# Performance work log

Hardware: AMD Instinct MI355X
Metric: run time of the kernel (lower is better)

The kernel has to match this reference:

```python
import jax, jax.numpy as jnp
import numpy as np

DIM = 1024
HEADS = 16
MLP = 4096

def setup_inputs() -> dict:
    key = jax.random.key(0)
    ks = jax.random.split(key, 8)
    s = 0.02
    return {
        "x": jax.random.normal(ks[0], (4, 2048, DIM), dtype=jnp.float32),
        "W_qkv": jax.random.normal(ks[1], (DIM, 3 * DIM), dtype=jnp.float32) * s,
        "W_o": jax.random.normal(ks[2], (DIM, DIM), dtype=jnp.float32) * s,
        "b_o": jnp.zeros((DIM,), dtype=jnp.float32),
        "g1": jnp.ones((DIM,), dtype=jnp.float32),
        "be1": jnp.zeros((DIM,), dtype=jnp.float32),
        "W1": jax.random.normal(ks[3], (DIM, MLP), dtype=jnp.float32) * s,
        "b1": jnp.zeros((MLP,), dtype=jnp.float32),
        "W2": jax.random.normal(ks[4], (MLP, DIM), dtype=jnp.float32) * s,
        "b2": jnp.zeros((DIM,), dtype=jnp.float32),
        "g2": jnp.ones((DIM,), dtype=jnp.float32),
        "be2": jnp.zeros((DIM,), dtype=jnp.float32),
    }

def _gelu(x):
    # GELU approx used in source: x * sigmoid(1.702 * x)
    return x * jax.nn.sigmoid(1.702 * x)

def _layernorm(x, g, b, eps=1e-5):
    mu = jnp.mean(x, axis=-1, keepdims=True)
    var = jnp.var(x, axis=-1, keepdims=True)
    return (x - mu) * jax.lax.rsqrt(var + eps) * g + b

def reference(x, W_qkv, W_o, b_o, g1, be1, W1, b1, W2, b2, g2, be2):
    b, n, d = x.shape
    h = HEADS
    hd = d // h
    scale = hd ** -0.5
    qkv = x @ W_qkv                               # [b,n,3d]
    q, k, v = jnp.split(qkv, 3, axis=-1)
    q = q.reshape(b, n, h, hd).transpose(0, 2, 1, 3)  # [b,h,n,hd]
    k = k.reshape(b, n, h, hd).transpose(0, 2, 1, 3)
    v = v.reshape(b, n, h, hd).transpose(0, 2, 1, 3)
    dots = jnp.einsum('bhid,bhjd->bhij', q, k) * scale  # [b,h,n,n]
    attn = jax.nn.softmax(dots, axis=-1)
    out = jnp.einsum('bhij,bhjd->bhid', attn, v)
    out = out.transpose(0, 2, 1, 3).reshape(b, n, d)
    out = out @ W_o + b_o
    x = _layernorm(x + out, g1, be1)
    ff = _gelu(x @ W1 + b1) @ W2 + b2
    x = _layernorm(x + ff, g2, be2)
    return x
```

## Files before the change

kernel.cpp:

```cpp
#include <hip/hip_runtime.h>

typedef unsigned short u16;
typedef __attribute__((ext_vector_type(4))) float f32x4;
typedef __attribute__((ext_vector_type(8))) __bf16 bf16x8;
typedef __attribute__((ext_vector_type(8))) unsigned short u16x8;
typedef __attribute__((ext_vector_type(4))) unsigned short u16x4;

__device__ __forceinline__ u16 f2bf(float f) {
  __bf16 h = (__bf16)f;
  union { __bf16 h; u16 u; } v; v.h = h;
  return v.u;
}

__device__ __forceinline__ float bf2f(u16 u) {
  union { unsigned u; float f; } v; v.u = ((unsigned)u) << 16;
  return v.f;
}

__device__ __forceinline__ void async16(const void* g, void* l) {
  __builtin_amdgcn_global_load_lds(
      (const __attribute__((address_space(1))) unsigned int*)g,
      (__attribute__((address_space(3))) unsigned int*)l, 16, 0, 0);
}

__device__ __forceinline__ void barrier_f() {
  asm volatile("" ::: "memory");
  __builtin_amdgcn_s_barrier();
  asm volatile("" ::: "memory");
}

__global__ __launch_bounds__(256) void cvt_f32_bf16(const float* __restrict__ in,
                                                    u16* __restrict__ out, int n4) {
  int i = blockIdx.x * 256 + threadIdx.x;
  if (i >= n4) return;
  f32x4 v = *(const f32x4*)(in + (long)i * 4);
  u16x4 o;
#pragma unroll
  for (int j = 0; j < 4; j++) o[j] = f2bf(v[j]);
  *(u16x4*)(out + (long)i * 4) = o;
}

__global__ __launch_bounds__(256) void transpose_cvt(const float* __restrict__ W,
                                                     u16* __restrict__ Wt, int K, int N) {
  __shared__ float tile[32][33];
  int n0 = blockIdx.x * 32, k0 = blockIdx.y * 32;
  int tx = threadIdx.x & 31, ty = threadIdx.x >> 5;
#pragma unroll
  for (int i = 0; i < 32; i += 8)
    tile[ty + i][tx] = W[(long)(k0 + ty + i) * N + n0 + tx];
  __syncthreads();
#pragma unroll
  for (int i = 0; i < 32; i += 8)
    Wt[(long)(n0 + ty + i) * K + k0 + tx] = f2bf(tile[tx][ty + i]);
}

template <int BIAS, int GELU, int OBF, int QSCALE, int VW, int SPLITK>
__global__ __launch_bounds__(512, 1) void gemm8p(const u16* __restrict__ A,
                                                 const u16* __restrict__ Bt,
                                                 void* __restrict__ Cp,
                                                 const float* __restrict__ bias,
                                                 u16* __restrict__ vt,
                                                 int M, int N, int Kst, int Klen) {
  __shared__ u16 As[2][256 * 64];
  __shared__ u16 Bs[2][256 * 64];
  const int t = threadIdx.x, wid = t >> 6, ln = t & 63;
  const int lr = ln & 15, lg = ln >> 4;
  const int wr = wid >> 2, wc = wid & 3;

  const int gx = gridDim.x, gy = gridDim.y;
  const int nwg = gx * gy * gridDim.z;
  const int flat = (blockIdx.z * gy + blockIdx.y) * gx + blockIdx.x;
  const int cpx = nwg >> 3;
  const int swz = (flat & 7) * cpx + (flat >> 3);
  const int sx = swz % gx, rest = swz / gx;
  const int sy = rest % gy, sz = rest / gy;
  const int m0 = sy * 256, n0 = sx * 256;
  const long zo = (long)sz * Klen;
  const int NT = Klen >> 6;

  const int srow = t >> 3;
  const int sch = ((t & 7) ^ (srow & 7)) * 8;
  const u16* gA = A + (long)(m0 + srow) * Kst + zo + sch;
  const u16* gB = Bt + (long)(n0 + srow) * Kst + zo + sch;
  const long KL = Kst;

#define STAGE_A(tt, h)                                                     \
  {                                                                        \
    const u16* s_ = gA + (long)((h) * 128) * KL + (long)(tt) * 64;         \
    char* d_ = (char*)As + ((tt) & 1) * 32768 + (h) * 16384 + wid * 1024;  \
    async16(s_, d_);                                                       \
    async16(s_ + 64 * KL, d_ + 8192);                                      \
  }
#define STAGE_B(tt, h)                                                     \
  {                                                                        \
    const u16* s_ = gB + (long)((h) * 128) * KL + (long)(tt) * 64;         \
    char* d_ = (char*)Bs + ((tt) & 1) * 32768 + (h) * 16384 + wid * 1024;  \
    async16(s_, d_);                                                       \
    async16(s_ + 64 * KL, d_ + 8192);                                      \
  }

  f32x4 acc[8][4] = {};
  const int cx0 = (lg ^ (lr & 7)) * 16;
  const int cx1 = ((4 + lg) ^ (lr & 7)) * 16;

  STAGE_A(0, 0); STAGE_A(0, 1);
  STAGE_B(0, 0); STAGE_B(0, 1);
  STAGE_A(1, 0); STAGE_A(1, 1);

  for (int tK = 0; tK < NT; ++tK) {
    const int cur = tK & 1;
    const char* ldsA = (const char*)As + cur * 32768;
    const char* ldsB = (const char*)Bs + cur * 32768;
    if (tK == NT - 1) {
      asm volatile("s_waitcnt vmcnt(0)" ::: "memory");
    } else {
      asm volatile("s_waitcnt vmcnt(4)" ::: "memory");
    }
    barrier_f();

    bf16x8 aLo[4][2], aHi[4][2], bLo[2][2], bHi[2][2];
#pragma unroll
    for (int mf = 0; mf < 4; mf++) {
      int row = wr * 128 + mf * 16 + lr;
      aLo[mf][0] = *(const bf16x8*)(ldsA + row * 128 + cx0);
      aLo[mf][1] = *(const bf16x8*)(ldsA + row * 128 + cx1);
    }
#pragma unroll
    for (int nf = 0; nf < 2; nf++) {
      int row = wc * 64 + nf * 16 + lr;
      bLo[nf][0] = *(const bf16x8*)(ldsB + row * 128 + cx0);
      bLo[nf][1] = *(const bf16x8*)(ldsB + row * 128 + cx1);
    }
    if (tK + 1 < NT) STAGE_B(tK + 1, 0);
    barrier_f();
    __builtin_amdgcn_s_setprio(1);
#pragma unroll
    for (int mf = 0; mf < 4; mf++)
#pragma unroll
      for (int nf = 0; nf < 2; nf++) {
        acc[mf][nf] = __builtin_amdgcn_mfma_f32_16x16x32_bf16(aLo[mf][0], bLo[nf][0], acc[mf][nf], 0, 0, 0);
        acc[mf][nf] = __builtin_amdgcn_mfma_f32_16x16x32_bf16(aLo[mf][1], bLo[nf][1], acc[mf][nf], 0, 0, 0);
      }
    __builtin_amdgcn_s_setprio(0);
    barrier_f();

#pragma unroll
    for (int mf = 0; mf < 4; mf++) {
      int row = wr * 128 + (mf + 4) * 16 + lr;
      aHi[mf][0] = *(const bf16x8*)(ldsA + row * 128 + cx0);
      aHi[mf][1] = *(const bf16x8*)(ldsA + row * 128 + cx1);
    }
    if (tK + 1 < NT) STAGE_B(tK + 1, 1);
    barrier_f();
    __builtin_amdgcn_s_setprio(1);
#pragma unroll
    for (int mf = 0; mf < 4; mf++)
#pragma unroll
      for (int nf = 0; nf < 2; nf++) {
        acc[mf + 4][nf] = __builtin_amdgcn_mfma_f32_16x16x32_bf16(aHi[mf][0], bLo[nf][0], acc[mf + 4][nf], 0, 0, 0);
        acc[mf + 4][nf] = __builtin_amdgcn_mfma_f32_16x16x32_bf16(aHi[mf][1], bLo[nf][1], acc[mf + 4][nf], 0, 0, 0);
      }
    __builtin_amdgcn_s_setprio(0);
    barrier_f();

#pragma unroll
    for (int nf = 0; nf < 2; nf++) {
      int row = wc * 64 + (nf + 2) * 16 + lr;
      bHi[nf][0] = *(const bf16x8*)(ldsB + row * 128 + cx0);
      bHi[nf][1] = *(const bf16x8*)(ldsB + row * 128 + cx1);
    }
    if (tK + 2 < NT) STAGE_A(tK + 2, 0);
    barrier_f();
    __builtin_amdgcn_s_setprio(1);
#pragma unroll
    for (int mf = 0; mf < 4; mf++)
#pragma unroll
      for (int nf = 0; nf < 2; nf++) {
        acc[mf][nf + 2] = __builtin_amdgcn_mfma_f32_16x16x32_bf16(aLo[mf][0], bHi[nf][0], acc[mf][nf + 2], 0, 0, 0);
        acc[mf][nf + 2] = __builtin_amdgcn_mfma_f32_16x16x32_bf16(aLo[mf][1], bHi[nf][1], acc[mf][nf + 2], 0, 0, 0);
      }
    __builtin_amdgcn_s_setprio(0);
    barrier_f();

    if (tK + 2 < NT) STAGE_A(tK + 2, 1);
    barrier_f();
    __builtin_amdgcn_s_setprio(1);
#pragma unroll
    for (int mf = 0; mf < 4; mf++)
#pragma unroll
      for (int nf = 0; nf < 2; nf++) {
        acc[mf + 4][nf + 2] = __builtin_amdgcn_mfma_f32_16x16x32_bf16(aHi[mf][0], bHi[nf][0], acc[mf + 4][nf + 2], 0, 0, 0);
        acc[mf + 4][nf + 2] = __builtin_amdgcn_mfma_f32_16x16x32_bf16(aHi[mf][1], bHi[nf][1], acc[mf + 4][nf + 2], 0, 0, 0);
      }
    __builtin_amdgcn_s_setprio(0);
    barrier_f();
  }
#undef STAGE_A
#undef STAGE_B

  u16* const Cu = (u16*)Cp + (SPLITK ? (long)sz * M * N : 0);
#pragma unroll
  for (int mf = 0; mf < 8; mf++) {
    int rbase = m0 + wr * 128 + mf * 16 + lg * 4;
#pragma unroll
    for (int nf = 0; nf < 4; nf++) {
      int col = n0 + wc * 64 + nf * 16 + lr;
      float bv = BIAS ? bias[col] : 0.f;
      if (VW && col >= 2048) {
        int hd = col - 2048;
        int bq = rbase >> 11, key = rbase & 2047;
        u16x4 o4;
#pragma unroll
        for (int r = 0; r < 4; r++) o4[r] = f2bf(acc[mf][nf][r]);
        *(u16x4*)&vt[((long)(bq * 16 + (hd >> 6)) * 64 + (hd & 63)) * 2048 + key] = o4;
      } else if (SPLITK) {
#pragma unroll
        for (int r = 0; r < 4; r++)
          Cu[(long)(rbase + r) * N + col] = f2bf(acc[mf][nf][r]);
      } else {
#pragma unroll
        for (int r = 0; r < 4; r++) {
          float v = acc[mf][nf][r] + bv;
          if (GELU) v = v / (1.f + __expf(-1.702f * v));
          if (QSCALE && col < 1024) v *= 0.18033688011112043f;
          if (OBF) ((u16*)Cp)[(long)(rbase + r) * N + col] = f2bf(v);
          else ((float*)Cp)[(long)(rbase + r) * N + col] = v;
        }
      }
    }
  }
}

__global__ __launch_bounds__(512, 6) void attn_kernel(const u16* __restrict__ qkv,
                                                      const u16* __restrict__ vt,
                                                      u16* __restrict__ out) {
  const int b = blockIdx.y >> 4, h = blockIdx.y & 15;
  const int q0 = blockIdx.x * 128;
  const int t = threadIdx.x, wv = t >> 6, ln = t & 63;
  const int lr = ln & 15, lg = ln >> 4;
  __shared__ u16 Ks[2][64 * 64];
  __shared__ u16 Vs[2][64 * 64];
  __shared__ u16 Pl[8][16 * 64];
  const long tok0 = (long)b * 2048;

  bf16x8 aQ[2];
  {
    long row = tok0 + q0 + wv * 16 + lr;
#pragma unroll
    for (int kf = 0; kf < 2; kf++)
      aQ[kf] = *(const bf16x8*)&qkv[row * 3072 + h * 64 + kf * 32 + lg * 8];
  }

  const int isK = (t < 256);
  const int tt = t & 255;
  const int sr = tt >> 3;
  const int sc = ((tt & 7) ^ (sr & 7)) * 8;
  const u16* gS = isK ? qkv + (tok0 + sr) * 3072 + 1024 + h * 64 + sc
                      : vt + ((long)(b * 16 + h) * 64 + sr) * 2048 + sc;
  const long src2 = isK ? (long)32 * 3072 : (long)32 * 2048;
  const long step = isK ? (long)64 * 3072 : 64;
  char* const dS = (isK ? (char*)&Ks[0][0] : (char*)&Vs[0][0]) + (wv & 3) * 1024;

  f32x4 accO[4] = {};
  f32x4 accL = {};

  bf16x8 bOnes;
  {
    union { u16x8 u; bf16x8 b; } ou;
#pragma unroll
    for (int j = 0; j < 8; j++) ou.u[j] = 0x3F80;
    bOnes = ou.b;
  }

  async16(gS, dS);
  async16(gS + src2, dS + 4096);
  const u16* gSn = gS + step;

  for (int it = 0; it < 32; ++it) {
    const int cur = it & 1;
    if (it < 31) {
      char* nS = dS + (cur ^ 1) * 8192;
      async16(gSn, nS);
      async16(gSn + src2, nS + 4096);
      gSn += step;
      asm volatile("s_waitcnt vmcnt(2)" ::: "memory");
    } else {
      asm volatile("s_waitcnt vmcnt(0)" ::: "memory");
    }
    __builtin_amdgcn_s_barrier();
    __builtin_amdgcn_sched_barrier(0);
    const u16* Kc = &Ks[cur][0];
    const u16* Vc = &Vs[cur][0];

    f32x4 accS[4];
    __builtin_amdgcn_s_setprio(1);
#pragma unroll
    for (int nc = 0; nc < 4; nc++) {
      f32x4 s = {};
#pragma unroll
      for (int kf = 0; kf < 2; kf++) {
        int krow = nc * 16 + lr;
        bf16x8 aK = *(const bf16x8*)&Kc[krow * 64 + ((kf * 32 + lg * 8) ^ ((krow & 7) << 3))];
        s = __builtin_amdgcn_mfma_f32_16x16x32_bf16(aK, aQ[kf], s, 0, 0, 0);
      }
      accS[nc] = s;
    }
    __builtin_amdgcn_s_setprio(0);

    u16x4 pw[4];
#pragma unroll
    for (int nc = 0; nc < 4; nc++) {
#pragma unroll
      for (int r = 0; r < 4; r++) pw[nc][r] = f2bf(exp2f(accS[nc][r]));
    }
#pragma unroll
    for (int nc = 0; nc < 4; nc++)
      *(u16x4*)&Pl[wv][lr * 64 + ((nc * 16 + lg * 4) ^ ((lr & 7) << 3))] = pw[nc];

    __builtin_amdgcn_s_setprio(1);
#pragma unroll
    for (int kf = 0; kf < 2; kf++) {
      bf16x8 aP = *(const bf16x8*)&Pl[wv][lr * 64 + ((kf * 32 + lg * 8) ^ ((lr & 7) << 3))];
      accL = __builtin_amdgcn_mfma_f32_16x16x32_bf16(aP, bOnes, accL, 0, 0, 0);
#pragma unroll
      for (int d = 0; d < 4; d++) {
        int vrow = d * 16 + lr;
        bf16x8 bV = *(const bf16x8*)&Vc[vrow * 64 + ((kf * 32 + lg * 8) ^ ((vrow & 7) << 3))];
        accO[d] = __builtin_amdgcn_mfma_f32_16x16x32_bf16(aP, bV, accO[d], 0, 0, 0);
      }
    }
    __builtin_amdgcn_s_setprio(0);
    __builtin_amdgcn_s_barrier();
    __builtin_amdgcn_sched_barrier(0);
  }

  float inv[4];
#pragma unroll
  for (int j = 0; j < 4; j++) inv[j] = 1.f / accL[j];
#pragma unroll
  for (int d = 0; d < 4; d++) {
#pragma unroll
    for (int j = 0; j < 4; j++) {
      float v = accO[d][j] * inv[j];
      out[(tok0 + q0 + wv * 16 + lg * 4 + j) * 1024 + h * 64 + d * 16 + lr] = f2bf(v);
    }
  }
}

template <int WB, int MODE>
__global__ __launch_bounds__(256) void ln_kernel(const float* __restrict__ xin,
                                                 const float* __restrict__ res,
                                                 const u16* __restrict__ p0,
                                                 const u16* __restrict__ p1,
                                                 const float* __restrict__ bias,
                                                 const float* __restrict__ g,
                                                 const float* __restrict__ be,
                                                 float* __restrict__ of,
                                                 u16* __restrict__ ob) {
  int row = blockIdx.x, t = threadIdx.x;
  long base = (long)row * 1024 + t * 4;
  f32x4 a = *(const f32x4*)(xin + base);
  f32x4 v;
  if (MODE == 0) {
    f32x4 bv = *(const f32x4*)(res + base);
    v = a + bv;
  } else {
    u16x4 u0 = *(const u16x4*)(p0 + base);
    u16x4 u1 = *(const u16x4*)(p1 + base);
    f32x4 bb4 = *(const f32x4*)(bias + t * 4);
#pragma unroll
    for (int j = 0; j < 4; j++) v[j] = a[j] + bf2f(u0[j]) + bf2f(u1[j]) + bb4[j];
  }
  float s = v[0] + v[1] + v[2] + v[3];
  float ss = v[0] * v[0] + v[1] * v[1] + v[2] * v[2] + v[3] * v[3];
#pragma unroll
  for (int o = 1; o < 64; o <<= 1) { s += __shfl_xor(s, o); ss += __shfl_xor(ss, o); }
  __shared__ float sm[8];
  if ((t & 63) == 0) { sm[t >> 6] = s; sm[4 + (t >> 6)] = ss; }
  __syncthreads();
  s = sm[0] + sm[1] + sm[2] + sm[3];
  ss = sm[4] + sm[5] + sm[6] + sm[7];
  float mu = s * 0.0009765625f;
  float var = ss * 0.0009765625f - mu * mu;
  float inv = rsqrtf(var + 1e-5f);
  f32x4 gg = *(const f32x4*)(g + t * 4);
  f32x4 bb = *(const f32x4*)(be + t * 4);
  f32x4 y;
#pragma unroll
  for (int j = 0; j < 4; j++) y[j] = (v[j] - mu) * inv * gg[j] + bb[j];
  *(f32x4*)(of + base) = y;
  if (WB) {
    u16x4 o4;
#pragma unroll
    for (int j = 0; j < 4; j++) o4[j] = f2bf(y[j]);
    *(u16x4*)(ob + base) = o4;
  }
}

extern "C" void kernel_launch(void* const* d_in, const int* in_sizes, int n_in,
                              void* d_out, int out_size, void* d_ws, size_t ws_size,
                              hipStream_t stream) {
  const float* x = (const float*)d_in[0];
  const float* Wqkv = (const float*)d_in[1];
  const float* Wo = (const float*)d_in[2];
  const float* bo = (const float*)d_in[3];
  const float* g1 = (const float*)d_in[4];
  const float* be1 = (const float*)d_in[5];
  const float* W1 = (const float*)d_in[6];
  const float* b1 = (const float*)d_in[7];
  const float* W2 = (const float*)d_in[8];
  const float* b2 = (const float*)d_in[9];
  const float* g2 = (const float*)d_in[10];
  const float* be2 = (const float*)d_in[11];
  float* out = (float*)d_out;
  char* ws = (char*)d_ws;

  u16* xb = (u16*)(ws + 0);
  u16* qkvb = (u16*)(ws + 16777216);
  u16* h1b = (u16*)(ws + 0);
  u16* vtb = (u16*)(ws + 67108864);
  u16* x1b = (u16*)(ws + 67108864);
  u16* attnb = (u16*)(ws + 83886080);
  float* x1f = (float*)(ws + 83886080);
  u16* pp = (u16*)(ws + 117440512);
  u16* ffp = (u16*)(ws + 117440512);
  u16* wqkvt = (u16*)(ws + 150994944);
  u16* wot = (u16*)(ws + 157286400);
  u16* w1t = (u16*)(ws + 159383552);
  u16* w2t = (u16*)(ws + 167772160);

  cvt_f32_bf16<<<8192, 256, 0, stream>>>(x, xb, 2097152);
  transpose_cvt<<<dim3(96, 32), 256, 0, stream>>>(Wqkv, wqkvt, 1024, 3072);
  transpose_cvt<<<dim3(32, 32), 256, 0, stream>>>(Wo, wot, 1024, 1024);
  transpose_cvt<<<dim3(128, 32), 256, 0, stream>>>(W1, w1t, 1024, 4096);
  transpose_cvt<<<dim3(32, 128), 256, 0, stream>>>(W2, w2t, 4096, 1024);
  gemm8p<0, 0, 1, 1, 1, 0><<<dim3(12, 32, 1), 512, 0, stream>>>(
      xb, wqkvt, qkvb, nullptr, vtb, 8192, 3072, 1024, 1024);
  attn_kernel<<<dim3(16, 64), 512, 0, stream>>>(qkvb, vtb, attnb);
  gemm8p<0, 0, 0, 0, 0, 1><<<dim3(4, 32, 2), 512, 0, stream>>>(
      attnb, wot, pp, nullptr, nullptr, 8192, 1024, 1024, 512);
  ln_kernel<1, 1><<<8192, 256, 0, stream>>>(x, nullptr, pp, pp + (long)8192 * 1024, bo,
                                            g1, be1, x1f, x1b);
  gemm8p<1, 1, 1, 0, 0, 0><<<dim3(16, 32, 1), 512, 0, stream>>>(
      x1b, w1t, h1b, b1, nullptr, 8192, 4096, 1024, 1024);
  gemm8p<0, 0, 0, 0, 0, 1><<<dim3(4, 32, 2), 512, 0, stream>>>(
      h1b, w2t, ffp, nullptr, nullptr, 8192, 1024, 4096, 2048);
  ln_kernel<0, 1><<<8192, 256, 0, stream>>>(x1f, nullptr, ffp, ffp + (long)8192 * 1024, b2,
                                            g2, be2, out, nullptr);
}
```

Measured before the change: 396.0 us.

## Rework attention with 32x32 MFMA, register-resident P, and pre-tiled K/V layouts

The QKV GEMM epilogue now writes Q (pre-scaled) to a separate buffer and writes K and V into blocked, pre-tiled layouts. The attention kernel can then stage them with contiguous async loads and no swizzling. Attention moves from 16x16x32 to 32x32x16 MFMAs with 256 queries per block. P stays in registers, exchanged across lanes by shuffles instead of going through LDS, and row sums are accumulated in scalar registers rather than by an MFMA against a ones vector. The second layernorm now reads the bf16 copy of x1 instead of an fp32 copy, which removes the fp32 intermediate write but lowers residual precision; the scattered element-wise K stores in the GEMM epilogue may also be costly.

```diff
diff --git a/kernel.cpp b/kernel.cpp
--- a/kernel.cpp
+++ b/kernel.cpp
@@ -1,7 +1,9 @@
 #include <hip/hip_runtime.h>
 
 typedef unsigned short u16;
+typedef unsigned int u32;
 typedef __attribute__((ext_vector_type(4))) float f32x4;
+typedef __attribute__((ext_vector_type(16))) float f32x16;
 typedef __attribute__((ext_vector_type(8))) __bf16 bf16x8;
 typedef __attribute__((ext_vector_type(8))) unsigned short u16x8;
 typedef __attribute__((ext_vector_type(4))) unsigned short u16x4;
@@ -15,6 +17,10 @@
 __device__ __forceinline__ float bf2f(u16 u) {
   union { unsigned u; float f; } v; v.u = ((unsigned)u) << 16;
   return v.f;
+}
+
+__device__ __forceinline__ u32 pk2(float a, float b) {
+  return (u32)f2bf(a) | ((u32)f2bf(b) << 16);
 }
 
 __device__ __forceinline__ void async16(const void* g, void* l) {
@@ -54,12 +60,13 @@
     Wt[(long)(n0 + ty + i) * K + k0 + tx] = f2bf(tile[tx][ty + i]);
 }
 
-template <int BIAS, int GELU, int OBF, int QSCALE, int VW, int SPLITK>
+template <int BIAS, int GELU, int OBF, int QKV, int SPLITK>
 __global__ __launch_bounds__(512, 1) void gemm8p(const u16* __restrict__ A,
                                                  const u16* __restrict__ Bt,
                                                  void* __restrict__ Cp,
                                                  const float* __restrict__ bias,
-                                                 u16* __restrict__ vt,
+                                                 u16* __restrict__ kt2,
+                                                 u16* __restrict__ vt2,
                                                  int M, int N, int Kst, int Klen) {
   __shared__ u16 As[2][256 * 64];
   __shared__ u16 Bs[2][256 * 64];
@@ -206,13 +213,28 @@
     for (int nf = 0; nf < 4; nf++) {
       int col = n0 + wc * 64 + nf * 16 + lr;
       float bv = BIAS ? bias[col] : 0.f;
-      if (VW && col >= 2048) {
-        int hd = col - 2048;
-        int bq = rbase >> 11, key = rbase & 2047;
-        u16x4 o4;
-#pragma unroll
-        for (int r = 0; r < 4; r++) o4[r] = f2bf(acc[mf][nf][r]);
-        *(u16x4*)&vt[((long)(bq * 16 + (hd >> 6)) * 64 + (hd & 63)) * 2048 + key] = o4;
+      if (QKV) {
+        int bq = rbase >> 11;
+        if (col < 1024) {
+#pragma unroll
+          for (int r = 0; r < 4; r++)
+            ((u16*)Cp)[(long)(rbase + r) * 1024 + col] = f2bf(acc[mf][nf][r] * 0.18033688011112043f);
+        } else if (col < 2048) {
+          int hd = col - 1024, h_ = hd >> 6, d = hd & 63;
+#pragma unroll
+          for (int r = 0; r < 4; r++) {
+            int key = (rbase + r) & 2047;
+            kt2[((((long)(bq * 16 + h_) * 32 + (key >> 6)) * 8 + (d >> 3)) * 64 + (key & 63)) * 8 + (d & 7)] =
+                f2bf(acc[mf][nf][r]);
+          }
+        } else {
+          int hd = col - 2048, h_ = hd >> 6, d = hd & 63;
+          int key0 = rbase & 2047;
+          u16x4 o4;
+#pragma unroll
+          for (int r = 0; r < 4; r++) o4[r] = f2bf(acc[mf][nf][r]);
+          *(u16x4*)&vt2[((((long)(bq * 16 + h_) * 32 + (key0 >> 6)) * 8 + ((key0 >> 3) & 7)) * 64 + d) * 8 + (key0 & 7)] = o4;
+        }
       } else if (SPLITK) {
 #pragma unroll
         for (int r = 0; r < 4; r++)
@@ -222,7 +244,6 @@
         for (int r = 0; r < 4; r++) {
           float v = acc[mf][nf][r] + bv;
           if (GELU) v = v / (1.f + __expf(-1.702f * v));
-          if (QSCALE && col < 1024) v *= 0.18033688011112043f;
           if (OBF) ((u16*)Cp)[(long)(rbase + r) * N + col] = f2bf(v);
           else ((float*)Cp)[(long)(rbase + r) * N + col] = v;
         }
@@ -231,58 +252,45 @@
   }
 }
 
-__global__ __launch_bounds__(512, 6) void attn_kernel(const u16* __restrict__ qkv,
-                                                      const u16* __restrict__ vt,
+__global__ __launch_bounds__(512, 4) void attn_kernel(const u16* __restrict__ qb,
+                                                      const u16* __restrict__ kt2,
+                                                      const u16* __restrict__ vt2,
                                                       u16* __restrict__ out) {
-  const int b = blockIdx.y >> 4, h = blockIdx.y & 15;
-  const int q0 = blockIdx.x * 128;
+  const int bh = blockIdx.y, h = bh & 15;
+  const int q0 = blockIdx.x * 256;
   const int t = threadIdx.x, wv = t >> 6, ln = t & 63;
-  const int lr = ln & 15, lg = ln >> 4;
-  __shared__ u16 Ks[2][64 * 64];
-  __shared__ u16 Vs[2][64 * 64];
-  __shared__ u16 Pl[8][16 * 64];
-  const long tok0 = (long)b * 2048;
-
-  bf16x8 aQ[2];
+  const int lq = ln & 31, hi = ln >> 5;
+  __shared__ u16 Ks[2][4096];
+  __shared__ u16 Vs[2][4096];
+  const long tok0 = (long)(bh >> 4) * 2048;
+
+  bf16x8 bQ[4];
   {
-    long row = tok0 + q0 + wv * 16 + lr;
-#pragma unroll
-    for (int kf = 0; kf < 2; kf++)
-      aQ[kf] = *(const bf16x8*)&qkv[row * 3072 + h * 64 + kf * 32 + lg * 8];
+    long row = tok0 + q0 + wv * 32 + lq;
+    const u16* qp = &qb[row * 1024 + h * 64 + hi * 8];
+#pragma unroll
+    for (int c = 0; c < 4; c++) bQ[c] = *(const bf16x8*)(qp + c * 16);
   }
 
   const int isK = (t < 256);
   const int tt = t & 255;
-  const int sr = tt >> 3;
-  const int sc = ((tt & 7) ^ (sr & 7)) * 8;
-  const u16* gS = isK ? qkv + (tok0 + sr) * 3072 + 1024 + h * 64 + sc
-                      : vt + ((long)(b * 16 + h) * 64 + sr) * 2048 + sc;
-  const long src2 = isK ? (long)32 * 3072 : (long)32 * 2048;
-  const long step = isK ? (long)64 * 3072 : 64;
+  const u16* gS = (isK ? kt2 : vt2) + (long)bh * 131072 + tt * 8;
   char* const dS = (isK ? (char*)&Ks[0][0] : (char*)&Vs[0][0]) + (wv & 3) * 1024;
 
-  f32x4 accO[4] = {};
-  f32x4 accL = {};
-
-  bf16x8 bOnes;
-  {
-    union { u16x8 u; bf16x8 b; } ou;
-#pragma unroll
-    for (int j = 0; j < 8; j++) ou.u[j] = 0x3F80;
-    bOnes = ou.b;
-  }
+  f32x16 accO0 = {}, accO1 = {};
+  float accLs = 0.f;
 
   async16(gS, dS);
-  async16(gS + src2, dS + 4096);
-  const u16* gSn = gS + step;
+  async16(gS + 2048, dS + 4096);
+  gS += 4096;
 
   for (int it = 0; it < 32; ++it) {
     const int cur = it & 1;
     if (it < 31) {
       char* nS = dS + (cur ^ 1) * 8192;
-      async16(gSn, nS);
-      async16(gSn + src2, nS + 4096);
-      gSn += step;
+      async16(gS, nS);
+      async16(gS + 2048, nS + 4096);
+      gS += 4096;
       asm volatile("s_waitcnt vmcnt(2)" ::: "memory");
     } else {
       asm volatile("s_waitcnt vmcnt(0)" ::: "memory");
@@ -292,64 +300,72 @@
     const u16* Kc = &Ks[cur][0];
     const u16* Vc = &Vs[cur][0];
 
-    f32x4 accS[4];
+    u32 frag[4][4];
+#pragma unroll
+    for (int kb = 0; kb < 2; kb++) {
+      f32x16 s = {};
+      __builtin_amdgcn_s_setprio(1);
+#pragma unroll
+      for (int c = 0; c < 4; c++) {
+        bf16x8 aK = *(const bf16x8*)&Kc[((c * 2 + hi) * 64 + kb * 32 + lq) * 8];
+        s = __builtin_amdgcn_mfma_f32_32x32x16_bf16(aK, bQ[c], s, 0, 0, 0);
+      }
+      __builtin_amdgcn_s_setprio(0);
+      float pv[16];
+#pragma unroll
+      for (int r = 0; r < 16; r++) { pv[r] = exp2f(s[r]); accLs += pv[r]; }
+#pragma unroll
+      for (int cc = 0; cc < 2; cc++) {
+        u32 dA0 = pk2(pv[8 * cc + 0], pv[8 * cc + 1]);
+        u32 dA1 = pk2(pv[8 * cc + 2], pv[8 * cc + 3]);
+        u32 dB0 = pk2(pv[8 * cc + 4], pv[8 * cc + 5]);
+        u32 dB1 = pk2(pv[8 * cc + 6], pv[8 * cc + 7]);
+        u32 e0 = (u32)__shfl_xor((int)dA0, 32);
+        u32 e1 = (u32)__shfl_xor((int)dA1, 32);
+        u32 f0 = (u32)__shfl_xor((int)dB0, 32);
+        u32 f1 = (u32)__shfl_xor((int)dB1, 32);
+        frag[kb * 2 + cc][0] = hi ? f0 : dA0;
+        frag[kb * 2 + cc][1] = hi ? f1 : dA1;
+        frag[kb * 2 + cc][2] = hi ? dB0 : e0;
+        frag[kb * 2 + cc][3] = hi ? dB1 : e1;
+      }
+    }
+
     __builtin_amdgcn_s_setprio(1);
 #pragma unroll
-    for (int nc = 0; nc < 4; nc++) {
-      f32x4 s = {};
-#pragma unroll
-      for (int kf = 0; kf < 2; kf++) {
-        int krow = nc * 16 + lr;
-        bf16x8 aK = *(const bf16x8*)&Kc[krow * 64 + ((kf * 32 + lg * 8) ^ ((krow & 7) << 3))];
-        s = __builtin_amdgcn_mfma_f32_16x16x32_bf16(aK, aQ[kf], s, 0, 0, 0);
-      }
-      accS[nc] = s;
-    }
-    __builtin_amdgcn_s_setprio(0);
-
-    u16x4 pw[4];
-#pragma unroll
-    for (int nc = 0; nc < 4; nc++) {
-#pragma unroll
-      for (int r = 0; r < 4; r++) pw[nc][r] = f2bf(exp2f(accS[nc][r]));
-    }
-#pragma unroll
-    for (int nc = 0; nc < 4; nc++)
-      *(u16x4*)&Pl[wv][lr * 64 + ((nc * 16 + lg * 4) ^ ((lr & 7) << 3))] = pw[nc];
-
-    __builtin_amdgcn_s_setprio(1);
-#pragma unroll
-    for (int kf = 0; kf < 2; kf++) {
-      bf16x8 aP = *(const bf16x8*)&Pl[wv][lr * 64 + ((kf * 32 + lg * 8) ^ ((lr & 7) << 3))];
-      accL = __builtin_amdgcn_mfma_f32_16x16x32_bf16(aP, bOnes, accL, 0, 0, 0);
-#pragma unroll
-      for (int d = 0; d < 4; d++) {
-        int vrow = d * 16 + lr;
-        bf16x8 bV = *(const bf16x8*)&Vc[vrow * 64 + ((kf * 32 + lg * 8) ^ ((vrow & 7) << 3))];
-        accO[d] = __builtin_amdgcn_mfma_f32_16x16x32_bf16(aP, bV, accO[d], 0, 0, 0);
-      }
+    for (int c2 = 0; c2 < 4; c2++) {
+      union { u32 u[4]; bf16x8 v; } pb;
+      pb.u[0] = frag[c2][0]; pb.u[1] = frag[c2][1];
+      pb.u[2] = frag[c2][2]; pb.u[3] = frag[c2][3];
+      bf16x8 aV0 = *(const bf16x8*)&Vc[((c2 * 2 + hi) * 64 + lq) * 8];
+      bf16x8 aV1 = *(const bf16x8*)&Vc[((c2 * 2 + hi) * 64 + 32 + lq) * 8];
+      accO0 = __builtin_amdgcn_mfma_f32_32x32x16_bf16(aV0, pb.v, accO0, 0, 0, 0);
+      accO1 = __builtin_amdgcn_mfma_f32_32x32x16_bf16(aV1, pb.v, accO1, 0, 0, 0);
     }
     __builtin_amdgcn_s_setprio(0);
     __builtin_amdgcn_s_barrier();
     __builtin_amdgcn_sched_barrier(0);
   }
 
-  float inv[4];
-#pragma unroll
-  for (int j = 0; j < 4; j++) inv[j] = 1.f / accL[j];
-#pragma unroll
-  for (int d = 0; d < 4; d++) {
+  float lT = accLs + __shfl_xor(accLs, 32);
+  float inv = 1.f / lT;
+  long tq = tok0 + q0 + wv * 32 + lq;
+  u16* op = &out[tq * 1024 + h * 64 + hi * 4];
+#pragma unroll
+  for (int qd = 0; qd < 4; qd++) {
+    u16x4 o4, o5;
 #pragma unroll
     for (int j = 0; j < 4; j++) {
-      float v = accO[d][j] * inv[j];
-      out[(tok0 + q0 + wv * 16 + lg * 4 + j) * 1024 + h * 64 + d * 16 + lr] = f2bf(v);
-    }
-  }
-}
-
-template <int WB, int MODE>
-__global__ __launch_bounds__(256) void ln_kernel(const float* __restrict__ xin,
-                                                 const float* __restrict__ res,
+      o4[j] = f2bf(accO0[qd * 4 + j] * inv);
+      o5[j] = f2bf(accO1[qd * 4 + j] * inv);
+    }
+    *(u16x4*)(op + qd * 8) = o4;
+    *(u16x4*)(op + 32 + qd * 8) = o5;
+  }
+}
+
+template <int XBF, int OF32>
+__global__ __launch_bounds__(256) void ln_kernel(const void* __restrict__ xin,
                                                  const u16* __restrict__ p0,
                                                  const u16* __restrict__ p1,
                                                  const float* __restrict__ bias,
@@ -359,18 +375,20 @@
                                                  u16* __restrict__ ob) {
   int row = blockIdx.x, t = threadIdx.x;
   long base = (long)row * 1024 + t * 4;
-  f32x4 a = *(const f32x4*)(xin + base);
+  f32x4 a;
+  if (XBF) {
+    u16x4 xa = *((const u16x4*)xin + row * 256 + t);
+#pragma unroll
+    for (int j = 0; j < 4; j++) a[j] = bf2f(xa[j]);
+  } else {
+    a = *((const f32x4*)xin + row * 256 + t);
+  }
+  u16x4 u0 = *(const u16x4*)(p0 + base);
+  u16x4 u1 = *(const u16x4*)(p1 + base);
+  f32x4 bb4 = *(const f32x4*)(bias + t * 4);
   f32x4 v;
-  if (MODE == 0) {
-    f32x4 bv = *(const f32x4*)(res + base);
-    v = a + bv;
-  } else {
-    u16x4 u0 = *(const u16x4*)(p0 + base);
-    u16x4 u1 = *(const u16x4*)(p1 + base);
-    f32x4 bb4 = *(const f32x4*)(bias + t * 4);
-#pragma unroll
-    for (int j = 0; j < 4; j++) v[j] = a[j] + bf2f(u0[j]) + bf2f(u1[j]) + bb4[j];
-  }
+#pragma unroll
+  for (int j = 0; j < 4; j++) v[j] = a[j] + bf2f(u0[j]) + bf2f(u1[j]) + bb4[j];
   float s = v[0] + v[1] + v[2] + v[3];
   float ss = v[0] * v[0] + v[1] * v[1] + v[2] * v[2] + v[3] * v[3];
 #pragma unroll
@@ -388,8 +406,9 @@
   f32x4 y;
 #pragma unroll
   for (int j = 0; j < 4; j++) y[j] = (v[j] - mu) * inv * gg[j] + bb[j];
-  *(f32x4*)(of + base) = y;
-  if (WB) {
+  if (OF32) {
+    *(f32x4*)(of + base) = y;
+  } else {
     u16x4 o4;
 #pragma unroll
     for (int j = 0; j < 4; j++) o4[j] = f2bf(y[j]);
@@ -416,35 +435,35 @@
   char* ws = (char*)d_ws;
 
   u16* xb = (u16*)(ws + 0);
-  u16* qkvb = (u16*)(ws + 16777216);
+  u16* qb = (u16*)(ws + 16777216);
+  u16* kt2b = (u16*)(ws + 33554432);
+  u16* vt2b = (u16*)(ws + 50331648);
   u16* h1b = (u16*)(ws + 0);
-  u16* vtb = (u16*)(ws + 67108864);
-  u16* x1b = (u16*)(ws + 67108864);
-  u16* attnb = (u16*)(ws + 83886080);
-  float* x1f = (float*)(ws + 83886080);
-  u16* pp = (u16*)(ws + 117440512);
-  u16* ffp = (u16*)(ws + 117440512);
-  u16* wqkvt = (u16*)(ws + 150994944);
-  u16* wot = (u16*)(ws + 157286400);
-  u16* w1t = (u16*)(ws + 159383552);
-  u16* w2t = (u16*)(ws + 167772160);
+  u16* attnb = (u16*)(ws + 67108864);
+  u16* x1b = (u16*)(ws + 83886080);
+  u16* pp = (u16*)(ws + 100663296);
+  u16* ffp = (u16*)(ws + 100663296);
+  u16* wqkvt = (u16*)(ws + 134217728);
+  u16* wot = (u16*)(ws + 140509184);
+  u16* w1t = (u16*)(ws + 142606336);
+  u16* w2t = (u16*)(ws + 150994944);
 
   cvt_f32_bf16<<<8192, 256, 0, stream>>>(x, xb, 2097152);
   transpose_cvt<<<dim3(96, 32), 256, 0, stream>>>(Wqkv, wqkvt, 1024, 3072);
   transpose_cvt<<<dim3(32, 32), 256, 0, stream>>>(Wo, wot, 1024, 1024);
   transpose_cvt<<<dim3(128, 32), 256, 0, stream>>>(W1, w1t, 1024, 4096);
   transpose_cvt<<<dim3(32, 128), 256, 0, stream>>>(W2, w2t, 4096, 1024);
-  gemm8p<0, 0, 1, 1, 1, 0><<<dim3(12, 32, 1), 512, 0, stream>>>(
-      xb, wqkvt, qkvb, nullptr, vtb, 8192, 3072, 1024, 1024);
-  attn_kernel<<<dim3(16, 64), 512, 0, stream>>>(qkvb, vtb, attnb);
-  gemm8p<0, 0, 0, 0, 0, 1><<<dim3(4, 32, 2), 512, 0, stream>>>(
-      attnb, wot, pp, nullptr, nullptr, 8192, 1024, 1024, 512);
-  ln_kernel<1, 1><<<8192, 256, 0, stream>>>(x, nullptr, pp, pp + (long)8192 * 1024, bo,
-                                            g1, be1, x1f, x1b);
-  gemm8p<1, 1, 1, 0, 0, 0><<<dim3(16, 32, 1), 512, 0, stream>>>(
-      x1b, w1t, h1b, b1, nullptr, 8192, 4096, 1024, 1024);
-  gemm8p<0, 0, 0, 0, 0, 1><<<dim3(4, 32, 2), 512, 0, stream>>>(
-      h1b, w2t, ffp, nullptr, nullptr, 8192, 1024, 4096, 2048);
-  ln_kernel<0, 1><<<8192, 256, 0, stream>>>(x1f, nullptr, ffp, ffp + (long)8192 * 1024, b2,
+  gemm8p<0, 0, 0, 1, 0><<<dim3(12, 32, 1), 512, 0, stream>>>(
+      xb, wqkvt, qb, nullptr, kt2b, vt2b, 8192, 3072, 1024, 1024);
+  attn_kernel<<<dim3(8, 64), 512, 0, stream>>>(qb, kt2b, vt2b, attnb);
+  gemm8p<0, 0, 0, 0, 1><<<dim3(4, 32, 2), 512, 0, stream>>>(
+      attnb, wot, pp, nullptr, nullptr, nullptr, 8192, 1024, 1024, 512);
+  ln_kernel<0, 0><<<8192, 256, 0, stream>>>(x, pp, pp + (long)8192 * 1024, bo,
+                                            g1, be1, nullptr, x1b);
+  gemm8p<1, 1, 1, 0, 0><<<dim3(16, 32, 1), 512, 0, stream>>>(
+      x1b, w1t, h1b, b1, nullptr, nullptr, 8192, 4096, 1024, 1024);
+  gemm8p<0, 0, 0, 0, 1><<<dim3(4, 32, 2), 512, 0, stream>>>(
+      h1b, w2t, ffp, nullptr, nullptr, nullptr, 8192, 1024, 4096, 2048);
+  ln_kernel<1, 1><<<8192, 256, 0, stream>>>(x1b, ffp, ffp + (long)8192 * 1024, b2,
                                             g2, be2, out, nullptr);
 }
```

After: 398.6 us. About the same (+0.6%).
